# Kernel tuning notes

Hardware: AMD Instinct MI355X
Metric: run time of the kernel (lower is better)

The kernel has to match this reference:

```python
import jax, jax.numpy as jnp
import numpy as np

B = 4      # cfg.TRAIN.IMS_PER_BATCH
P = 256    # proposals per image (equal per image; all labels > 0)
C = 151    # cfg.MODEL.NUM_CLASSES
R = 51     # cfg.MODEL.NUM_RELATIONS
W = 0.5    # cfg.REL_INFER.NONE_BGREL_WEIGHT


def setup_inputs() -> dict:
    key = jax.random.key(0)
    k1, k2, k3, k4 = jax.random.split(key, 4)
    roi_scores = jax.random.normal(k1, (B * P, C), dtype=jnp.float32)
    rel_scores = jax.random.normal(k2, (B * P * P, R), dtype=jnp.float32)
    roi_labels = jax.random.randint(k3, (B * P,), 1, C, dtype=jnp.int32)  # labels > 0 (fg only)
    # sparse relation co-occurrence matrix densified; background relation slice set to 1
    relationship_mat = (jax.random.uniform(k4, (C, C, R)) < 0.05).astype(jnp.float32)
    relationship_mat = relationship_mat.at[:, :, 0].set(1.0)
    return {
        "roi_scores": roi_scores,
        "rel_scores": rel_scores,
        "relationship_mat": relationship_mat,
        "roi_labels": roi_labels,
        "num_images": B,
    }


def reference(roi_scores, rel_scores, relationship_mat, roi_labels, num_images):
    nb = num_images
    p = roi_scores.shape[0] // nb
    rel = rel_scores.reshape(nb, p, p, -1)          # [B, P, P, R]
    labels = roi_labels.reshape(nb, p)              # [B, P]
    # computed in the original forward but unused by the returned loss
    _unary = jax.nn.log_softmax(roi_scores, axis=1)
    off_diag = (1.0 - jnp.eye(p, dtype=roi_scores.dtype))  # zero out p == q pairs

    def per_image(lab, rl):
        # lab: [P] int, rl: [P, P, R]
        A = relationship_mat[lab]        # [P, C, R]  rows gathered by subject label
        At = relationship_mat[:, lab]    # [C, P, R]  cols gathered by subject label
        # b[p,q,c] = A[p,c,0]*rl[p,q,0] + W * sum_{r>=1} A[p,c,r]*rl[p,q,r]
        b = A[:, None, :, 0] * rl[:, :, None, 0] \
            + W * jnp.einsum('pcr,pqr->pqc', A[..., 1:], rl[..., 1:])
        # t[p,q,c] = At[c,p,0]*rl[q,p,0] + W * sum_{r>=1} At[c,p,r]*rl[q,p,r]
        t = At[..., 0].T[:, None, :] * rl[..., 0].T[:, :, None] \
            + W * jnp.einsum('cpr,qpr->pqc', At[..., 1:], rl[..., 1:])
        theta = 0.5 * (b + t) * off_diag[:, :, None]  # mask diagonal pairs
        theta = theta.sum(0)                          # sum over partner p -> [P, C]
        logp = jax.nn.log_softmax(theta, axis=1)
        return -logp[jnp.arange(p), lab]              # [P]

    loss = jax.vmap(per_image)(labels, rel)           # [B, P]
    return loss.mean()
```

## Files before the change

### kernel.cpp

```cpp
#include <hip/hip_runtime.h>
#include <math.h>

#define NB 4
#define PP 256
#define CC 151
#define RR 51
#define CM 160
#define KS 64
#define NROW (NB*PP)
#define MLB 10240
#define NRELROW (NB*PP*PP)
#define CONVB (NRELROW/8)
#define PREPB (CC*2)

typedef _Float16 half8 __attribute__((ext_vector_type(8)));
typedef _Float16 half2v __attribute__((ext_vector_type(2)));
typedef float floatx16 __attribute__((ext_vector_type(16)));

#define OFF_M1 ((size_t)0)
#define OFF_M2 (OFF_M1 + (size_t)CC*MLB*2)
#define OFF_PT (OFF_M2 + (size_t)CC*MLB*2)
#define OFF_R16 (OFF_PT + (size_t)KS*NROW*CM*4)

__global__ __launch_bounds__(256) void prep_kernel(const float* __restrict__ M,
                                                   const float* __restrict__ rel,
                                                   _Float16* __restrict__ m1,
                                                   _Float16* __restrict__ m2,
                                                   _Float16* __restrict__ rel16,
                                                   float* __restrict__ out) {
    const int bid = blockIdx.x;
    if (bid < PREPB) {
        const int l = (bid < CC) ? bid : bid - CC;
        const int mat = (bid < CC) ? 0 : 1;
        if (bid == 0 && threadIdx.x == 0) *out = 0.f;
        _Float16* dst = (mat ? m2 : m1) + (size_t)l * MLB;
        for (int e = threadIdx.x; e < MLB; e += 256) {
            int oct = e / 1280;
            int rem = e - oct * 1280;
            int c = rem >> 3, j = rem & 7;
            int r = oct * 8 + j;
            float v = 0.f;
            if (r < RR && c < CC) {
                size_t src = ((size_t)(mat ? c * CC + l : l * CC + c)) * RR + r;
                v = (r == 0 ? 0.5f : 0.25f) * M[src];
            }
            dst[e] = (_Float16)v;
        }
    } else {
        const int t = threadIdx.x;
        const size_t row = (size_t)(bid - PREPB) * 8 + (t >> 5);
        const int d  = t & 31;
        const int h0 = 2 * d;
        const int a  = ((int)row >> 8) & 255;
        const int b  = (int)row & 255;
        const bool live = (a != b);
        const float* src = rel + row * RR;
        float v0 = (live && h0 < RR)     ? src[h0]     : 0.f;
        float v1 = (live && h0 + 1 < RR) ? src[h0 + 1] : 0.f;
        half2v p;
        p[0] = (_Float16)v0;
        p[1] = (_Float16)v1;
        *(half2v*)(rel16 + row * 64 + h0) = p;
    }
}

__global__ __launch_bounds__(256) void gemm_kernel(const _Float16* __restrict__ rel16,
                                                   const _Float16* __restrict__ m1,
                                                   const _Float16* __restrict__ m2,
                                                   const int* __restrict__ labels,
                                                   float* __restrict__ part) {
    __shared__ _Float16 Bt[2][2560];
    const int tid  = threadIdx.x;
    const int ks   = blockIdx.x & 63;
    const int rbk  = (blockIdx.x >> 6) & 1;
    const int n    = blockIdx.x >> 7;
    const int wave = tid >> 6, lane = tid & 63;
    const int m32  = lane & 31, kh = lane >> 5;
    const int i0   = ks * 4;
    const int rowimg = rbk * 128 + wave * 32 + m32;

    int labs[4];
    #pragma unroll
    for (int j = 0; j < 4; ++j) labs[j] = labels[n * PP + i0 + j];

    floatx16 acc[5];
    #pragma unroll
    for (int ct = 0; ct < 5; ++ct)
        #pragma unroll
        for (int r2 = 0; r2 < 16; ++r2) acc[ct][r2] = 0.f;

    auto stageB = [&](int h, int buf) {
        const int il = h >> 3, mh = (h >> 2) & 1, t = h & 3;
        const _Float16* base = (mh ? m2 : m1) + (size_t)labs[il] * MLB + t * 2560;
        #pragma unroll
        for (int j = 0; j < 2; ++j) {
            int s = j * 256 + tid;
            if (s < 320) {
                __builtin_amdgcn_global_load_lds(
                    (const __attribute__((address_space(1))) unsigned int*)(base + s * 8),
                    (__attribute__((address_space(3))) unsigned int*)(&Bt[buf][(size_t)s * 8]),
                    16, 0, 0);
            }
        }
    };
    auto loadA = [&](int h, half8* a) {
        const int il = h >> 3, mh = (h >> 2) & 1, t = h & 3;
        const int i = i0 + il;
        const size_t row = mh ? ((size_t)(n * PP + rowimg) * PP + i)
                              : ((size_t)(n * PP + i) * PP + rowimg);
        *a = *(const half8*)(rel16 + row * 64 + t * 16 + kh * 8);
    };

    stageB(0, 0);
    half8 av;
    loadA(0, &av);

    #pragma unroll 2
    for (int h = 0; h < 32; ++h) {
        __syncthreads();
        if (h < 31) stageB(h + 1, (h + 1) & 1);
        half8 avn;
        if (h < 31) loadA(h + 1, &avn);

        const _Float16* bb = &Bt[h & 1][(size_t)(kh * 160 + m32) * 8];
        #pragma unroll
        for (int ct = 0; ct < 5; ++ct) {
            half8 b = *(const half8*)(bb + ct * 256);
            acc[ct] = __builtin_amdgcn_mfma_f32_32x32x16_f16(av, b, acc[ct], 0, 0, 0);
        }
        av = avn;
    }

    float* pb = part + ((size_t)ks * NROW + n * PP + rbk * 128 + wave * 32) * CM;
    #pragma unroll
    for (int ct = 0; ct < 5; ++ct)
        #pragma unroll
        for (int reg = 0; reg < 16; ++reg) {
            int row = (reg & 3) + 8 * (reg >> 2) + 4 * kh;
            pb[(size_t)row * CM + ct * 32 + m32] = acc[ct][reg];
        }
}

__global__ __launch_bounds__(256) void reduce_loss_kernel(const float* __restrict__ part,
                                                          const int* __restrict__ labels,
                                                          float* __restrict__ out) {
    __shared__ float th[CM];
    const int row = blockIdx.x;
    const int t = threadIdx.x;
    if (t < CM) {
        float s = 0.f;
        #pragma unroll
        for (int ks = 0; ks < KS; ++ks)
            s += part[((size_t)ks * NROW + row) * CM + t];
        th[t] = s;
    }
    __syncthreads();
    if (t < 64) {
        float v0 = (t < CC)       ? th[t]       : -INFINITY;
        float v1 = (t + 64 < CC)  ? th[t + 64]  : -INFINITY;
        float v2 = (t + 128 < CC) ? th[t + 128] : -INFINITY;
        float m = fmaxf(v0, fmaxf(v1, v2));
        #pragma unroll
        for (int o = 32; o > 0; o >>= 1) m = fmaxf(m, __shfl_xor(m, o, 64));
        float s = 0.f;
        if (t < CC)       s += expf(v0 - m);
        if (t + 64 < CC)  s += expf(v1 - m);
        if (t + 128 < CC) s += expf(v2 - m);
        #pragma unroll
        for (int o = 32; o > 0; o >>= 1) s += __shfl_xor(s, o, 64);
        if (t == 0) {
            atomicAdd(out, (m + logf(s) - th[labels[row]]) * (1.0f / NROW));
        }
    }
}

extern "C" void kernel_launch(void* const* d_in, const int* in_sizes, int n_in,
                              void* d_out, int out_size, void* d_ws, size_t ws_size,
                              hipStream_t stream) {
    const float* rel    = (const float*)d_in[1];
    const float* relmat = (const float*)d_in[2];
    const int*   labels = (const int*)d_in[3];
    float* out = (float*)d_out;
    char* ws = (char*)d_ws;

    _Float16* m1    = (_Float16*)(ws + OFF_M1);
    _Float16* m2    = (_Float16*)(ws + OFF_M2);
    float*    part  = (float*)(ws + OFF_PT);
    _Float16* rel16 = (_Float16*)(ws + OFF_R16);

    prep_kernel<<<PREPB + CONVB, 256, 0, stream>>>(relmat, rel, m1, m2, rel16, out);
    gemm_kernel<<<NB * 2 * KS, 256, 0, stream>>>(rel16, m1, m2, labels, part);
    reduce_loss_kernel<<<NROW, 256, 0, stream>>>(part, labels, out);
}
```

Baseline: 166.3 us.

## Deepen GEMM prefetch pipeline to four LDS buffers and row-major partials

The GEMM kernel now uses four LDS buffers with a prefetch distance of two steps. The per-step __syncthreads is replaced by explicit vmcnt waits plus s_barrier, so global-to-LDS copies and A-fragment loads for later steps stay in flight during the current MFMAs. B staging is reissued as one 16-byte and one 4-byte direct-to-LDS load per thread, and the partial-sum buffer is reordered to [row][ks][c] so the reduce kernel reads contiguous memory. The trade-off is more LDS, fully unrolled code with hand-counted waits that can break if the compiler reorders memory ops, and more scattered stores in the GEMM epilogue.

Result: faster. 149.8 us (-9.9%).

```diff
diff --git a/kernel.cpp b/kernel.cpp
--- a/kernel.cpp
+++ b/kernel.cpp
@@ -20,7 +20,7 @@
 #define OFF_M1 ((size_t)0)
 #define OFF_M2 (OFF_M1 + (size_t)CC*MLB*2)
 #define OFF_PT (OFF_M2 + (size_t)CC*MLB*2)
-#define OFF_R16 (OFF_PT + (size_t)KS*NROW*CM*4)
+#define OFF_R16 (OFF_PT + (size_t)NROW*KS*CM*4)
 
 __global__ __launch_bounds__(256) void prep_kernel(const float* __restrict__ M,
                                                    const float* __restrict__ rel,
@@ -69,7 +69,7 @@
                                                    const _Float16* __restrict__ m2,
                                                    const int* __restrict__ labels,
                                                    float* __restrict__ part) {
-    __shared__ _Float16 Bt[2][2560];
+    __shared__ _Float16 Bt[4][2560];
     const int tid  = threadIdx.x;
     const int ks   = blockIdx.x & 63;
     const int rbk  = (blockIdx.x >> 6) & 1;
@@ -89,55 +89,56 @@
         #pragma unroll
         for (int r2 = 0; r2 < 16; ++r2) acc[ct][r2] = 0.f;
 
+    half8 aS[4];
+
     auto stageB = [&](int h, int buf) {
         const int il = h >> 3, mh = (h >> 2) & 1, t = h & 3;
         const _Float16* base = (mh ? m2 : m1) + (size_t)labs[il] * MLB + t * 2560;
-        #pragma unroll
-        for (int j = 0; j < 2; ++j) {
-            int s = j * 256 + tid;
-            if (s < 320) {
-                __builtin_amdgcn_global_load_lds(
-                    (const __attribute__((address_space(1))) unsigned int*)(base + s * 8),
-                    (__attribute__((address_space(3))) unsigned int*)(&Bt[buf][(size_t)s * 8]),
-                    16, 0, 0);
-            }
-        }
+        __builtin_amdgcn_global_load_lds(
+            (const __attribute__((address_space(1))) unsigned int*)(base + tid * 8),
+            (__attribute__((address_space(3))) unsigned int*)(&Bt[buf][tid * 8]),
+            16, 0, 0);
+        __builtin_amdgcn_global_load_lds(
+            (const __attribute__((address_space(1))) unsigned int*)(base + 2048 + tid * 2),
+            (__attribute__((address_space(3))) unsigned int*)(&Bt[buf][2048 + tid * 2]),
+            4, 0, 0);
     };
-    auto loadA = [&](int h, half8* a) {
+    auto loadA = [&](int h) {
         const int il = h >> 3, mh = (h >> 2) & 1, t = h & 3;
         const int i = i0 + il;
         const size_t row = mh ? ((size_t)(n * PP + rowimg) * PP + i)
                               : ((size_t)(n * PP + i) * PP + rowimg);
-        *a = *(const half8*)(rel16 + row * 64 + t * 16 + kh * 8);
+        aS[h & 3] = *(const half8*)(rel16 + row * 64 + t * 16 + kh * 8);
     };
-
-    stageB(0, 0);
-    half8 av;
-    loadA(0, &av);
-
-    #pragma unroll 2
-    for (int h = 0; h < 32; ++h) {
-        __syncthreads();
-        if (h < 31) stageB(h + 1, (h + 1) & 1);
-        half8 avn;
-        if (h < 31) loadA(h + 1, &avn);
-
-        const _Float16* bb = &Bt[h & 1][(size_t)(kh * 160 + m32) * 8];
+    auto computeStep = [&](int h) {
+        const _Float16* bb = &Bt[h & 3][(size_t)(kh * 160 + m32) * 8];
         #pragma unroll
         for (int ct = 0; ct < 5; ++ct) {
             half8 b = *(const half8*)(bb + ct * 256);
-            acc[ct] = __builtin_amdgcn_mfma_f32_32x32x16_f16(av, b, acc[ct], 0, 0, 0);
+            acc[ct] = __builtin_amdgcn_mfma_f32_32x32x16_f16(aS[h & 3], b, acc[ct], 0, 0, 0);
         }
-        av = avn;
+    };
+
+    stageB(0, 0); loadA(0);
+    stageB(1, 1); loadA(1);
+
+    #pragma unroll
+    for (int h = 0; h < 32; ++h) {
+        if (h + 2 < 32) { stageB(h + 2, (h + 2) & 3); loadA(h + 2); }
+        if (h < 30)       asm volatile("s_waitcnt vmcnt(6)" ::: "memory");
+        else if (h == 30) asm volatile("s_waitcnt vmcnt(3)" ::: "memory");
+        else              asm volatile("s_waitcnt vmcnt(0)" ::: "memory");
+        __builtin_amdgcn_s_barrier();
+        computeStep(h);
     }
 
-    float* pb = part + ((size_t)ks * NROW + n * PP + rbk * 128 + wave * 32) * CM;
+    float* pb = part + ((size_t)(n * PP + rbk * 128 + wave * 32) * KS + ks) * CM;
     #pragma unroll
     for (int ct = 0; ct < 5; ++ct)
         #pragma unroll
         for (int reg = 0; reg < 16; ++reg) {
             int row = (reg & 3) + 8 * (reg >> 2) + 4 * kh;
-            pb[(size_t)row * CM + ct * 32 + m32] = acc[ct][reg];
+            pb[(size_t)row * KS * CM + ct * 32 + m32] = acc[ct][reg];
         }
 }
 
@@ -148,10 +149,11 @@
     const int row = blockIdx.x;
     const int t = threadIdx.x;
     if (t < CM) {
+        const float* p = part + (size_t)row * KS * CM + t;
         float s = 0.f;
         #pragma unroll
         for (int ks = 0; ks < KS; ++ks)
-            s += part[((size_t)ks * NROW + row) * CM + t];
+            s += p[ks * CM];
         th[t] = s;
     }
     __syncthreads();
```
